# Optimization experiments

Measured on AMD Instinct MI355X. Metric: run time of the kernel, lower is better.

Reference implementation:

```python
import jax, jax.numpy as jnp
import numpy as np

L, B, C, OUT = 4, 4, 256, 4
H, W = 128, 128
HEADS, DH, G = 8, 32, 64
N = H * W
INNER = HEADS * DH
HID = 4 * C


def _ln(x, w, b, eps=1e-5):
    m = jnp.mean(x, -1, keepdims=True)
    v = jnp.mean((x - m) ** 2, -1, keepdims=True)
    return (x - m) / jnp.sqrt(v + eps) * w + b


def setup_inputs() -> dict:
    key = jax.random.key(0)
    ks = iter(jax.random.split(key, 16))
    nrm = lambda shape, s=0.02: jax.random.normal(next(ks), shape, jnp.float32) * s
    return dict(
        fx=jax.random.normal(next(ks), (B, N, C), jnp.float32),
        ln1_w=jnp.ones((L, C)), ln1_b=jnp.zeros((L, C)),
        convx_w=nrm((L, 3, 3, C, INNER)), convx_b=jnp.zeros((L, INNER)),
        convfx_w=nrm((L, 3, 3, C, INNER)), convfx_b=jnp.zeros((L, INNER)),
        slice_w=nrm((L, DH, G)), slice_b=jnp.zeros((L, G)),
        temperature=0.5 * jnp.ones((L, HEADS)),
        wq=nrm((L, DH, DH)), wk=nrm((L, DH, DH)), wv=nrm((L, DH, DH)),
        wo=nrm((L, INNER, C)), bo=jnp.zeros((L, C)),
        ln2_w=jnp.ones((L, C)), ln2_b=jnp.zeros((L, C)),
        w1=nrm((L, C, HID)), b1=jnp.zeros((L, HID)),
        w2=nrm((L, HID, C)), b2=jnp.zeros((L, C)),
        ln3_w=jnp.ones((C,)), ln3_b=jnp.zeros((C,)),
        w_out=nrm((C, OUT)), b_out=jnp.zeros((OUT,)),
    )


def reference(fx, ln1_w, ln1_b, convx_w, convx_b, convfx_w, convfx_b,
              slice_w, slice_b, temperature, wq, wk, wv, wo, bo,
              ln2_w, ln2_b, w1, b1, w2, b2, ln3_w, ln3_b, w_out, b_out):
    Bb = fx.shape[0]
    scale = DH ** -0.5
    for i in range(L):
        # --- Physics attention (slice attention) ---
        x = _ln(fx, ln1_w[i], ln1_b[i])
        ximg = x.reshape(Bb, H, W, C)  # NHWC
        conv = lambda w, b: jax.lax.conv_general_dilated(
            ximg, w, (1, 1), 'SAME',
            dimension_numbers=('NHWC', 'HWIO', 'NHWC')) + b
        fx_mid = conv(convfx_w[i], convfx_b[i]).reshape(Bb, N, HEADS, DH).transpose(0, 2, 1, 3)  # [B,h,N,d]
        x_mid = conv(convx_w[i], convx_b[i]).reshape(Bb, N, HEADS, DH).transpose(0, 2, 1, 3)
        temp = jnp.clip(temperature[i], 0.1, 5.0)[None, :, None, None]
        logits = (jnp.einsum('bhnd,dg->bhng', x_mid, slice_w[i]) + slice_b[i]) / temp
        sw = jax.nn.softmax(logits, axis=-1)  # [B,h,N,G]
        norm = sw.sum(2)  # [B,h,G]
        st = jnp.einsum('bhnc,bhng->bhgc', fx_mid, sw) / (norm + 1e-5)[..., None]  # [B,h,G,d]
        q = jnp.einsum('bhgc,cd->bhgd', st, wq[i])
        k = jnp.einsum('bhgc,cd->bhgd', st, wk[i])
        v = jnp.einsum('bhgc,cd->bhgd', st, wv[i])
        attn = jax.nn.softmax(jnp.einsum('bhgd,bhkd->bhgk', q, k) * scale, axis=-1)
        ot = jnp.einsum('bhgk,bhkd->bhgd', attn, v)  # [B,h,G,d]
        out_x = jnp.einsum('bhgc,bhng->bhnc', ot, sw)  # deslice back to points
        out_x = out_x.transpose(0, 2, 1, 3).reshape(Bb, N, INNER)
        fx = fx + out_x @ wo[i] + bo[i]
        # --- MLP (n_layers=0, no res inside) ---
        h = _ln(fx, ln2_w[i], ln2_b[i])
        h = jax.nn.gelu(h @ w1[i] + b1[i], approximate=False) @ w2[i] + b2[i]
        fx = fx + h
    # last-layer head
    return _ln(fx, ln3_w, ln3_b) @ w_out + b_out
```

## Files before the change

### kernel.cpp

```cpp
#include <hip/hip_runtime.h>
#include <hip/hip_bf16.h>

typedef __hip_bfloat16 bf16;
typedef __bf16 bfv8 __attribute__((ext_vector_type(8)));
typedef float f32x4 __attribute__((ext_vector_type(4)));

#define BB 4
#define HH 128
#define WWI 128
#define NN 16384
#define CC 256
#define LL 4
#define NHEADS 8
#define DHD 32
#define GG 64
#define INNERC 256
#define HIDD 1024
#define SPLIT 32
#define SSP 16

__device__ __forceinline__ float b2f(bf16 x) { return __bfloat162float(x); }
__device__ __forceinline__ bf16 f2b(float x) { return __float2bfloat16(x); }
__device__ __forceinline__ float us2f(unsigned short v) {
  return __uint_as_float(((unsigned)v) << 16);
}

__device__ __forceinline__ void async16(void* l, const void* g) {
  __builtin_amdgcn_global_load_lds(
      (const __attribute__((address_space(1))) void*)g,
      (__attribute__((address_space(3))) void*)l, 16, 0, 0);
}

__device__ __forceinline__ float wave_sum(float v) {
#pragma unroll
  for (int off = 32; off > 0; off >>= 1) v += __shfl_down(v, off, 64);
  return v;
}

__device__ __forceinline__ float gelu_exact(float x) {
  return 0.5f * x * (1.0f + erff(x * 0.70710678118654752f));
}

__global__ void transpose_cast_kernel(const float* __restrict__ src, bf16* __restrict__ dst,
                                      int R, int Cm) {
  __shared__ float tile[32][33];
  int tb = blockIdx.z;
  const float* s = src + (size_t)tb * R * Cm;
  bf16* d = dst + (size_t)tb * R * Cm;
  int c0 = blockIdx.x * 32, r0 = blockIdx.y * 32;
  int tx = threadIdx.x & 31, ty = threadIdx.x >> 5;
  for (int rr = ty; rr < 32; rr += 8) {
    int r = r0 + rr, c = c0 + tx;
    tile[rr][tx] = (r < R && c < Cm) ? s[(size_t)r * Cm + c] : 0.f;
  }
  __syncthreads();
  for (int cc = ty; cc < 32; cc += 8) {
    int c = c0 + cc, r = r0 + tx;
    if (c < Cm && r < R) d[(size_t)c * R + r] = f2b(tile[tx][cc]);
  }
}

__global__ void ln_kernel(const float* __restrict__ x, const float* __restrict__ w,
                          const float* __restrict__ b, bf16* __restrict__ out) {
  int pp = blockIdx.x;
  int t = threadIdx.x;
  float v = x[(size_t)pp * CC + t];
  float s = wave_sum(v);
  float sq = wave_sum(v * v);
  __shared__ float ls[4], lq[4];
  int wid = t >> 6, lane = t & 63;
  if (lane == 0) { ls[wid] = s; lq[wid] = sq; }
  __syncthreads();
  float tot = ls[0] + ls[1] + ls[2] + ls[3];
  float totq = lq[0] + lq[1] + lq[2] + lq[3];
  float mean = tot * (1.0f / CC);
  float var = totq * (1.0f / CC) - mean * mean;
  float rstd = rsqrtf(var + 1e-5f);
  float o = (v - mean) * rstd * w[t] + b[t];
  out[(size_t)pp * CC + t] = f2b(o);
}

__global__ __launch_bounds__(512) void conv_mfma_kernel(
    const bf16* __restrict__ xln, const bf16* __restrict__ wt,
    const float* __restrict__ bias, bf16* __restrict__ out,
    const float* __restrict__ zbuf) {
  __shared__ __align__(16) unsigned short As[3 * 130 * 64];
  __shared__ __align__(16) unsigned short Bsm[2][256 * 64];
  int bid = blockIdx.x;
  bid = (bid & 7) * 64 + (bid >> 3);
  int h = bid & 127;
  int b = bid >> 7;
  int t = threadIdx.x, lane = t & 63, wid = t >> 6;
  int wm = (wid & 1) * 64, wn = (wid >> 1) * 64;
  int l15 = lane & 15, l4 = lane >> 4;
  int wu = t & ~63;
  f32x4 acc[4][4];
#pragma unroll
  for (int mi = 0; mi < 4; ++mi)
#pragma unroll
    for (int ni = 0; ni < 4; ++ni) acc[mi][ni] = (f32x4){0.f, 0.f, 0.f, 0.f};
  const bf16* xbase = xln + (size_t)b * NN * CC;

  for (int q = 0; q < 4; ++q) {
#pragma unroll
    for (int k = 0; k < 6; ++k) {
      int u = t + k * 512;
      int jp = u & 7, pc = u >> 3;
      int r = pc / 130, cl = pc - r * 130;
      int j = jp ^ (cl & 7);
      int gr = h + r - 1, gc = cl - 1;
      const void* src =
          ((unsigned)gr < 128u && (unsigned)gc < 128u)
              ? (const void*)(xbase + ((size_t)(gr * WWI + gc)) * CC + q * 64 + j * 8)
              : (const void*)zbuf;
      async16(&As[(size_t)(wu + k * 512) * 8], src);
    }
    if (t < 48) {
      int u = t + 3072;
      int jp = u & 7, pc = u >> 3;
      int r = pc / 130, cl = pc - r * 130;
      int j = jp ^ (cl & 7);
      int gr = h + r - 1, gc = cl - 1;
      uint4 v = make_uint4(0u, 0u, 0u, 0u);
      if ((unsigned)gr < 128u && (unsigned)gc < 128u)
        v = *(const uint4*)(xbase + ((size_t)(gr * WWI + gc)) * CC + q * 64 + j * 8);
      *(uint4*)(&As[(size_t)u * 8]) = v;
    }
#pragma unroll
    for (int k = 0; k < 4; ++k) {
      int u = t + k * 512;
      int n = u >> 3, jp = u & 7, j = jp ^ (n & 7);
      async16(&Bsm[0][(size_t)(wu + k * 512) * 8],
              wt + (size_t)n * 256 + q * 64 + j * 8);
    }
    __syncthreads();

    for (int tap = 0; tap < 9; ++tap) {
      int cur = tap & 1;
      if (tap < 8) {
#pragma unroll
        for (int k = 0; k < 4; ++k) {
          int u = t + k * 512;
          int n = u >> 3, jp = u & 7, j = jp ^ (n & 7);
          async16(&Bsm[cur ^ 1][(size_t)(wu + k * 512) * 8],
                  wt + ((size_t)((tap + 1) * 256 + n)) * 256 + q * 64 + j * 8);
        }
      }
      int ky = tap / 3, kx = tap - ky * 3;
      const unsigned short* Bc = Bsm[cur];
#pragma unroll
      for (int s = 0; s < 2; ++s) {
        bfv8 af[4], bfr[4];
#pragma unroll
        for (int mi = 0; mi < 4; ++mi) {
          int cl = wm + mi * 16 + l15 + kx;
          af[mi] = *(const bfv8*)(&As[((size_t)(ky * 130 + cl)) * 64 +
                                      (((s * 4 + l4) ^ (cl & 7)) << 3)]);
        }
#pragma unroll
        for (int ni = 0; ni < 4; ++ni) {
          int rn = wn + ni * 16 + l15;
          bfr[ni] = *(const bfv8*)(&Bc[(size_t)rn * 64 + (((s * 4 + l4) ^ (rn & 7)) << 3)]);
        }
#pragma unroll
        for (int mi = 0; mi < 4; ++mi)
#pragma unroll
          for (int ni = 0; ni < 4; ++ni)
            acc[mi][ni] = __builtin_amdgcn_mfma_f32_16x16x32_bf16(af[mi], bfr[ni], acc[mi][ni], 0, 0, 0);
      }
      __syncthreads();
    }
  }
  int colB = wn + l15;
  int rowB = wm + l4 * 4;
#pragma unroll
  for (int ni = 0; ni < 4; ++ni) {
    int oc = colB + ni * 16;
    float bv = bias[oc];
#pragma unroll
    for (int mi = 0; mi < 4; ++mi) {
#pragma unroll
      for (int r = 0; r < 4; ++r) {
        int pix = rowB + mi * 16 + r;
        out[((size_t)(b * NN + h * WWI + pix)) * CC + oc] = f2b(acc[mi][ni][r] + bv);
      }
    }
  }
}

__global__ __launch_bounds__(256, 2) void gemm_acc_kernel(
    const bf16* __restrict__ A, const bf16* __restrict__ BT,
    const float* __restrict__ bias, float* __restrict__ outf,
    int M, int N, int K, size_t strideAz, size_t strideBz, size_t strideOz) {
  A  += (size_t)blockIdx.z * strideAz;
  BT += (size_t)blockIdx.z * strideBz;
  __shared__ __align__(16) unsigned short As[128 * 64];
  __shared__ __align__(16) unsigned short Bs[128 * 64];
  int m0 = blockIdx.x * 128, n0 = blockIdx.y * 128;
  int t = threadIdx.x, lane = t & 63, wid = t >> 6;
  int wm = (wid >> 1) * 64, wn = (wid & 1) * 64;
  int l15 = lane & 15, q4 = lane >> 4;
  int wg = wm >> 4, ng = wn >> 4;
  f32x4 acc[4][4];
#pragma unroll
  for (int mi = 0; mi < 4; ++mi)
#pragma unroll
    for (int ni = 0; ni < 4; ++ni) acc[mi][ni] = (f32x4){0.f, 0.f, 0.f, 0.f};

  for (int kb = 0; kb < K; kb += 64) {
    __syncthreads();
#pragma unroll
    for (int i = 0; i < 4; ++i) {
      int inst = wid * 4 + i;
      int g = inst >> 1, h2 = inst & 1;
      int row = g * 16 + l15;
      int kc = (h2 * 4 + q4) * 8;
      async16(&As[(size_t)g * 1024 + h2 * 512], A + (size_t)(m0 + row) * K + kb + kc);
      async16(&Bs[(size_t)g * 1024 + h2 * 512], BT + (size_t)(n0 + row) * K + kb + kc);
    }
    __syncthreads();
#pragma unroll
    for (int s = 0; s < 2; ++s) {
      int kgrp = s * 4 + q4;
      bfv8 af[4], bfr[4];
#pragma unroll
      for (int mi = 0; mi < 4; ++mi)
        af[mi] = *(const bfv8*)(&As[(size_t)(wg + mi) * 1024 + kgrp * 128 + l15 * 8]);
#pragma unroll
      for (int ni = 0; ni < 4; ++ni)
        bfr[ni] = *(const bfv8*)(&Bs[(size_t)(ng + ni) * 1024 + kgrp * 128 + l15 * 8]);
#pragma unroll
      for (int mi = 0; mi < 4; ++mi)
#pragma unroll
        for (int ni = 0; ni < 4; ++ni)
          acc[mi][ni] = __builtin_amdgcn_mfma_f32_16x16x32_bf16(af[mi], bfr[ni], acc[mi][ni], 0, 0, 0);
    }
  }
  int colB = n0 + wn + l15;
  int rowB = m0 + wm + q4 * 4;
#pragma unroll
  for (int ni = 0; ni < 4; ++ni) {
    int col = colB + ni * 16;
    float bv = bias[col];
#pragma unroll
    for (int mi = 0; mi < 4; ++mi) {
#pragma unroll
      for (int r = 0; r < 4; ++r) {
        int row = rowB + mi * 16 + r;
        outf[(size_t)blockIdx.z * strideOz + (size_t)row * N + col] += acc[mi][ni][r] + bv;
      }
    }
  }
}

__global__ __launch_bounds__(512) void mlp_fused_kernel(
    const bf16* __restrict__ xln, const bf16* __restrict__ w1t,
    const float* __restrict__ b1, const bf16* __restrict__ w2t,
    const float* __restrict__ b2, float* __restrict__ fx) {
  __shared__ __align__(16) unsigned short As[64 * 256];
  __shared__ __align__(16) bf16 Hs[64 * 128];
  __shared__ __align__(16) unsigned short Wb[128 * 256];
  int m0 = blockIdx.x * 64;
  int t = threadIdx.x, lane = t & 63, wid = t >> 6;
  int l15 = lane & 15, q4 = lane >> 4;
  int wm2 = (wid & 1) * 32, wn2 = (wid >> 1) * 32;
  int wm = (wid & 1) * 32, wn = (wid >> 1) * 64;
  int wu = t & ~63;

  const unsigned short* xg = (const unsigned short*)xln + (size_t)m0 * 256;
#pragma unroll
  for (int i = 0; i < 4; ++i) {
    int u = t + i * 512;
    int row = u >> 5;
    int su = (u & ~7) | ((u & 7) ^ (row & 7));
    async16(&As[(size_t)(wu + i * 512) * 8], xg + (size_t)su * 8);
  }
#pragma unroll
  for (int i = 0; i < 8; ++i) {
    int u = t + i * 512;
    int n = u >> 5, v = u & 31;
    int sv = (v & ~7) | ((v & 7) ^ (n & 7));
    async16(&Wb[(size_t)(wu + i * 512) * 8], w1t + (size_t)n * 256 + sv * 8);
  }

  f32x4 accO[2][4];
#pragma unroll
  for (int mi = 0; mi < 2; ++mi)
#pragma unroll
    for (int ni = 0; ni < 4; ++ni) accO[mi][ni] = (f32x4){0.f, 0.f, 0.f, 0.f};
  __syncthreads();

  for (int j = 0; j < 8; ++j) {
    int hbase = j * 128;
    f32x4 acc2[2][2];
#pragma unroll
    for (int mi = 0; mi < 2; ++mi)
#pragma unroll
      for (int nj = 0; nj < 2; ++nj) acc2[mi][nj] = (f32x4){0.f, 0.f, 0.f, 0.f};
#pragma unroll
    for (int kb = 0; kb < 4; ++kb) {
#pragma unroll
      for (int ks = 0; ks < 2; ++ks) {
        int kgrp = ks * 4 + q4;
        bfv8 af[2], bfr[2];
#pragma unroll
        for (int mi = 0; mi < 2; ++mi) {
          int row = wm2 + mi * 16 + l15;
          af[mi] = *(const bfv8*)(&As[row * 256 + kb * 64 + ((kgrp ^ (row & 7)) << 3)]);
        }
#pragma unroll
        for (int nj = 0; nj < 2; ++nj) {
          int n = wn2 + nj * 16 + l15;
          bfr[nj] = *(const bfv8*)(&Wb[n * 256 + kb * 64 + ((kgrp ^ (n & 7)) << 3)]);
        }
#pragma unroll
        for (int mi = 0; mi < 2; ++mi)
#pragma unroll
          for (int nj = 0; nj < 2; ++nj)
            acc2[mi][nj] = __builtin_amdgcn_mfma_f32_16x16x32_bf16(af[mi], bfr[nj], acc2[mi][nj], 0, 0, 0);
      }
    }
    __syncthreads();
#pragma unroll
    for (int i = 0; i < 8; ++i) {
      int u = t + i * 512;
      int n = u >> 4, v = u & 15;
      int sv = (v & ~7) | ((v & 7) ^ (n & 7));
      async16(&Wb[(size_t)(wu + i * 512) * 8], w2t + (size_t)n * 1024 + hbase + sv * 8);
    }
#pragma unroll
    for (int nj = 0; nj < 2; ++nj) {
      int coln = wn2 + nj * 16 + l15;
      float bv = b1[hbase + coln];
      int half = coln >> 6, sub = (coln >> 3) & 7, lo = coln & 7;
#pragma unroll
      for (int mi = 0; mi < 2; ++mi) {
#pragma unroll
        for (int r = 0; r < 4; ++r) {
          int row = wm2 + mi * 16 + q4 * 4 + r;
          float v = acc2[mi][nj][r] + bv;
          Hs[row * 128 + half * 64 + (((sub ^ (row & 7)) << 3) + lo)] = f2b(gelu_exact(v));
        }
      }
    }
    __syncthreads();
#pragma unroll
    for (int kb2 = 0; kb2 < 2; ++kb2) {
#pragma unroll
      for (int ks = 0; ks < 2; ++ks) {
        int kgrp = ks * 4 + q4;
        bfv8 af[2], bfr[4];
#pragma unroll
        for (int mi = 0; mi < 2; ++mi) {
          int row = wm + mi * 16 + l15;
          af[mi] = *(const bfv8*)(&Hs[row * 128 + kb2 * 64 + ((kgrp ^ (row & 7)) << 3)]);
        }
#pragma unroll
        for (int ni = 0; ni < 4; ++ni) {
          int n = wn + ni * 16 + l15;
          bfr[ni] = *(const bfv8*)(&Wb[n * 128 + kb2 * 64 + ((kgrp ^ (n & 7)) << 3)]);
        }
#pragma unroll
        for (int mi = 0; mi < 2; ++mi)
#pragma unroll
          for (int ni = 0; ni < 4; ++ni)
            accO[mi][ni] = __builtin_amdgcn_mfma_f32_16x16x32_bf16(af[mi], bfr[ni], accO[mi][ni], 0, 0, 0);
      }
    }
    if (j < 7) {
      __syncthreads();
#pragma unroll
      for (int i = 0; i < 8; ++i) {
        int u = t + i * 512;
        int n = u >> 5, v = u & 31;
        int sv = (v & ~7) | ((v & 7) ^ (n & 7));
        async16(&Wb[(size_t)(wu + i * 512) * 8],
                w1t + (size_t)(hbase + 128 + n) * 256 + sv * 8);
      }
      __syncthreads();
    }
  }
#pragma unroll
  for (int ni = 0; ni < 4; ++ni) {
    int col = wn + ni * 16 + l15;
    float bv = b2[col];
#pragma unroll
    for (int mi = 0; mi < 2; ++mi) {
#pragma unroll
      for (int r = 0; r < 4; ++r) {
        int row = m0 + wm + mi * 16 + q4 * 4 + r;
        fx[(size_t)row * 256 + col] += accO[mi][ni][r] + bv;
      }
    }
  }
}

__global__ __launch_bounds__(256) void slice_softmax_kernel(
    const bf16* __restrict__ xmid, const float* __restrict__ sw_w,
    const float* __restrict__ sw_b, const float* __restrict__ temp,
    bf16* __restrict__ swout) {
  __shared__ float wsm[32][64];
  __shared__ float xm[SSP][256];
  __shared__ float bias_s[64];
  __shared__ float rtc[8];
  int p0 = blockIdx.x * SSP;
  int t = threadIdx.x;
  for (int i = t; i < 2048; i += 256) wsm[i >> 6][i & 63] = sw_w[i];
  if (t < 64) bias_s[t] = sw_b[t];
  if (t < 8) {
    float x = temp[t];
    rtc[t] = 1.0f / fminf(fmaxf(x, 0.1f), 5.0f);
  }
  const unsigned short* xg = (const unsigned short*)xmid + (size_t)p0 * 256;
#pragma unroll
  for (int i2 = t; i2 < SSP * 32; i2 += 256) {
    uint4 v = ((const uint4*)xg)[i2];
    int p = i2 >> 5, c = (i2 & 31) << 3;
    xm[p][c + 0] = us2f((unsigned short)(v.x & 0xffff));
    xm[p][c + 1] = us2f((unsigned short)(v.x >> 16));
    xm[p][c + 2] = us2f((unsigned short)(v.y & 0xffff));
    xm[p][c + 3] = us2f((unsigned short)(v.y >> 16));
    xm[p][c + 4] = us2f((unsigned short)(v.z & 0xffff));
    xm[p][c + 5] = us2f((unsigned short)(v.z >> 16));
    xm[p][c + 6] = us2f((unsigned short)(v.w & 0xffff));
    xm[p][c + 7] = us2f((unsigned short)(v.w >> 16));
  }
  __syncthreads();
  int g = t & 63, pq = t >> 6;
  for (int pp2 = 0; pp2 < SSP / 4; ++pp2) {
    int p = pp2 * 4 + pq;
#pragma unroll
    for (int h = 0; h < NHEADS; ++h) {
      float acc = bias_s[g];
      const float* xr = &xm[p][h * 32];
#pragma unroll
      for (int d = 0; d < 32; ++d) acc += xr[d] * wsm[d][g];
      float logit = acc * rtc[h];
      float m = logit;
#pragma unroll
      for (int off = 32; off > 0; off >>= 1) m = fmaxf(m, __shfl_xor(m, off, 64));
      float e = __expf(logit - m);
      float s = e;
#pragma unroll
      for (int off = 32; off > 0; off >>= 1) s += __shfl_xor(s, off, 64);
      swout[(size_t)(p0 + p) * 512 + h * 64 + g] = f2b(e / s);
    }
  }
}

__global__ __launch_bounds__(256) void slice_st_kernel(
    const bf16* __restrict__ fxmid, const bf16* __restrict__ sw,
    float* __restrict__ stp, float* __restrict__ normp) {
  __shared__ __align__(16) unsigned short sw_s[64 * 64];
  __shared__ __align__(16) unsigned short fx_s[32 * 64];
  __shared__ float npart[2][64];
  int split = blockIdx.x, h = blockIdx.y, b = blockIdx.z;
  int t = threadIdx.x, w = t >> 6, lane = t & 63;
  int l15 = lane & 15, q4 = lane >> 4;
  int ns0 = split * (NN / SPLIT);
  const int NT = (NN / SPLIT) / 64;
  f32x4 acc0 = {0.f, 0.f, 0.f, 0.f}, acc1 = {0.f, 0.f, 0.f, 0.f};
  float nacc = 0.f;
  const unsigned short* swg = (const unsigned short*)sw + (size_t)b * NN * 512 + h * 64;
  const unsigned short* fxg = (const unsigned short*)fxmid + (size_t)b * NN * 256 + h * 32;

  for (int kt = 0; kt < NT; ++kt) {
    int n0 = ns0 + kt * 64;
    __syncthreads();
    if (w < 2) {
      int g = lane;
#pragma unroll
      for (int i = 0; i < 4; ++i) {
        int j = w + 2 * i;
        const unsigned short* p = swg + (size_t)(n0 + j * 8) * 512 + g;
        unsigned short v0 = p[0],     v1 = p[512],  v2 = p[1024], v3 = p[1536];
        unsigned short v4 = p[2048],  v5 = p[2560], v6 = p[3072], v7 = p[3584];
        nacc += us2f(v0) + us2f(v1) + us2f(v2) + us2f(v3) +
                us2f(v4) + us2f(v5) + us2f(v6) + us2f(v7);
        uint4 pk = make_uint4((unsigned)v0 | ((unsigned)v1 << 16),
                              (unsigned)v2 | ((unsigned)v3 << 16),
                              (unsigned)v4 | ((unsigned)v5 << 16),
                              (unsigned)v6 | ((unsigned)v7 << 16));
        ((uint4*)sw_s)[g * 8 + (j ^ (g & 7))] = pk;
      }
    } else {
      int d = lane & 31, nh = lane >> 5, w3 = w - 2;
#pragma unroll
      for (int i = 0; i < 2; ++i) {
        int nbase = (w3 * 2 + i) * 16 + nh * 8;
        const unsigned short* p = fxg + (size_t)(n0 + nbase) * 256 + d;
        unsigned short v0 = p[0],    v1 = p[256],  v2 = p[512],  v3 = p[768];
        unsigned short v4 = p[1024], v5 = p[1280], v6 = p[1536], v7 = p[1792];
        uint4 pk = make_uint4((unsigned)v0 | ((unsigned)v1 << 16),
                              (unsigned)v2 | ((unsigned)v3 << 16),
                              (unsigned)v4 | ((unsigned)v5 << 16),
                              (unsigned)v6 | ((unsigned)v7 << 16));
        int u = nbase >> 3;
        ((uint4*)fx_s)[d * 8 + (u ^ (d & 7))] = pk;
      }
    }
    __syncthreads();
    int gg = w * 16 + l15;
    int d0 = l15, d1 = 16 + l15;
#pragma unroll
    for (int ks = 0; ks < 2; ++ks) {
      bfv8 af  = ((const bfv8*)sw_s)[gg * 8 + ((ks * 4 + q4) ^ (gg & 7))];
      bfv8 bf0 = ((const bfv8*)fx_s)[d0 * 8 + ((ks * 4 + q4) ^ (d0 & 7))];
      bfv8 bf1 = ((const bfv8*)fx_s)[d1 * 8 + ((ks * 4 + q4) ^ (d1 & 7))];
      acc0 = __builtin_amdgcn_mfma_f32_16x16x32_bf16(af, bf0, acc0, 0, 0, 0);
      acc1 = __builtin_amdgcn_mfma_f32_16x16x32_bf16(af, bf1, acc1, 0, 0, 0);
    }
  }
  if (w < 2) npart[w][lane] = nacc;
  __syncthreads();
  int bh = b * NHEADS + h;
  if (t < 64) normp[(size_t)split * (BB * NHEADS * GG) + bh * 64 + t] = npart[0][t] + npart[1][t];
  size_t base = ((size_t)split * (BB * NHEADS * GG) + bh * 64) * 32;
#pragma unroll
  for (int r = 0; r < 4; ++r) {
    int g = w * 16 + q4 * 4 + r;
    stp[base + (size_t)g * 32 + l15] = acc0[r];
    stp[base + (size_t)g * 32 + 16 + l15] = acc1[r];
  }
}

__global__ __launch_bounds__(256) void attn_kernel(
    const float* __restrict__ stp, const float* __restrict__ normp,
    const float* __restrict__ wq, const float* __restrict__ wk,
    const float* __restrict__ wv, float* __restrict__ ot) {
  __shared__ float wqs[32 * 32], wks[32 * 32], wvs[32 * 32];
  __shared__ float st[GG][DHD + 1];
  __shared__ float qq[GG][DHD + 1], kk[GG][DHD + 1], vv[GG][DHD + 1];
  __shared__ float pm[GG][GG + 1];
  __shared__ float nrm[GG];
  int bh = blockIdx.x;
  int t = threadIdx.x;
  ((float4*)wqs)[t] = ((const float4*)wq)[t];
  ((float4*)wks)[t] = ((const float4*)wk)[t];
  ((float4*)wvs)[t] = ((const float4*)wv)[t];
  if (t < 64) {
    float ns = 0.f;
    for (int s = 0; s < SPLIT; ++s) ns += normp[(size_t)s * (BB * NHEADS * GG) + bh * 64 + t];
    nrm[t] = 1.0f / (ns + 1e-5f);
  }
  __syncthreads();
#pragma unroll
  for (int i = 0; i < 8; ++i) {
    int idx = t + i * 256;
    int g = idx >> 5, d = idx & 31;
    float a = 0.f;
    for (int s = 0; s < SPLIT; ++s)
      a += stp[((size_t)s * (BB * NHEADS * GG) + bh * 64 + g) * 32 + d];
    st[g][d] = a * nrm[g];
  }
  __syncthreads();
#pragma unroll
  for (int i = 0; i < 8; ++i) {
    int idx = t + i * 256;
    int g = idx >> 5, d = idx & 31;
    float aq = 0.f, ak = 0.f, av = 0.f;
#pragma unroll
    for (int c = 0; c < 32; ++c) {
      float sv = st[g][c];
      aq += sv * wqs[c * 32 + d];
      ak += sv * wks[c * 32 + d];
      av += sv * wvs[c * 32 + d];
    }
    qq[g][d] = aq; kk[g][d] = ak; vv[g][d] = av;
  }
  __syncthreads();
  {
    int g = t >> 2, sub = t & 3;
    float sc[16];
    float m = -1e30f;
    const float scale = 0.17677669529663687f;
#pragma unroll
    for (int jj = 0; jj < 16; ++jj) {
      int j = sub * 16 + jj;
      float a = 0.f;
#pragma unroll
      for (int d = 0; d < 32; ++d) a += qq[g][d] * kk[j][d];
      a *= scale;
      sc[jj] = a;
      m = fmaxf(m, a);
    }
    m = fmaxf(m, __shfl_xor(m, 1, 64));
    m = fmaxf(m, __shfl_xor(m, 2, 64));
    float ssum = 0.f;
#pragma unroll
    for (int jj = 0; jj < 16; ++jj) { sc[jj] = __expf(sc[jj] - m); ssum += sc[jj]; }
    ssum += __shfl_xor(ssum, 1, 64);
    ssum += __shfl_xor(ssum, 2, 64);
    float rs = 1.0f / ssum;
#pragma unroll
    for (int jj = 0; jj < 16; ++jj) pm[g][sub * 16 + jj] = sc[jj] * rs;
  }
  __syncthreads();
#pragma unroll
  for (int i = 0; i < 8; ++i) {
    int idx = t + i * 256;
    int g = idx >> 5, d = idx & 31;
    float a = 0.f;
#pragma unroll
    for (int j = 0; j < GG; ++j) a += pm[g][j] * vv[j][d];
    ot[((size_t)bh * GG + g) * DHD + d] = a;
  }
}

__global__ __launch_bounds__(256) void wc_kernel(const float* __restrict__ ot,
                                                 const float* __restrict__ wo,
                                                 bf16* __restrict__ wct) {
  __shared__ float ots[GG][DHD];
  int bh = blockIdx.x;
  int h = bh & 7, b = bh >> 3;
  int t = threadIdx.x;
  for (int i = t; i < GG * DHD; i += 256) ots[i >> 5][i & 31] = ot[(size_t)bh * (GG * DHD) + i];
  float wol[DHD];
#pragma unroll
  for (int d = 0; d < DHD; ++d) wol[d] = wo[(size_t)(h * DHD + d) * CC + t];
  __syncthreads();
  bf16* dst = wct + ((size_t)b * CC + t) * (NHEADS * GG) + h * GG;
#pragma unroll 4
  for (int g = 0; g < GG; ++g) {
    float a = 0.f;
#pragma unroll
    for (int d = 0; d < DHD; ++d) a += wol[d] * ots[g][d];
    dst[g] = f2b(a);
  }
}

__global__ void head_kernel(const float* __restrict__ fx, const float* __restrict__ w,
                            const float* __restrict__ b, const float* __restrict__ wout,
                            const float* __restrict__ bout, float* __restrict__ out) {
  int pp = blockIdx.x;
  int t = threadIdx.x;
  float v = fx[(size_t)pp * CC + t];
  float s = wave_sum(v);
  float sq = wave_sum(v * v);
  __shared__ float ls[4], lq[4];
  int wid = t >> 6, lane = t & 63;
  if (lane == 0) { ls[wid] = s; lq[wid] = sq; }
  __syncthreads();
  float tot = ls[0] + ls[1] + ls[2] + ls[3];
  float totq = lq[0] + lq[1] + lq[2] + lq[3];
  float mean = tot * (1.0f / CC);
  float var = totq * (1.0f / CC) - mean * mean;
  float rstd = rsqrtf(var + 1e-5f);
  float xn = (v - mean) * rstd * w[t] + b[t];
  __shared__ float xs[CC];
  xs[t] = xn;
  __syncthreads();
  if (t < 4) {
    float a = bout[t];
    for (int c = 0; c < CC; ++c) a += xs[c] * wout[c * 4 + t];
    out[(size_t)pp * 4 + t] = a;
  }
}

extern "C" void kernel_launch(void* const* d_in, const int* in_sizes, int n_in,
                              void* d_out, int out_size, void* d_ws, size_t ws_size,
                              hipStream_t stream) {
  const float* fx_in      = (const float*)d_in[0];
  const float* ln1_w      = (const float*)d_in[1];
  const float* ln1_b      = (const float*)d_in[2];
  const float* convx_w    = (const float*)d_in[3];
  const float* convx_b    = (const float*)d_in[4];
  const float* convfx_w   = (const float*)d_in[5];
  const float* convfx_b   = (const float*)d_in[6];
  const float* slice_w    = (const float*)d_in[7];
  const float* slice_b    = (const float*)d_in[8];
  const float* temperature= (const float*)d_in[9];
  const float* wq         = (const float*)d_in[10];
  const float* wk         = (const float*)d_in[11];
  const float* wv         = (const float*)d_in[12];
  const float* wo         = (const float*)d_in[13];
  const float* bo         = (const float*)d_in[14];
  const float* ln2_w      = (const float*)d_in[15];
  const float* ln2_b      = (const float*)d_in[16];
  const float* w1         = (const float*)d_in[17];
  const float* b1         = (const float*)d_in[18];
  const float* w2         = (const float*)d_in[19];
  const float* b2         = (const float*)d_in[20];
  const float* ln3_w      = (const float*)d_in[21];
  const float* ln3_b      = (const float*)d_in[22];
  const float* w_out      = (const float*)d_in[23];
  const float* b_out      = (const float*)d_in[24];
  float* out = (float*)d_out;

  char* ws = (char*)d_ws;
  size_t off = 0;
  auto alloc = [&](size_t bytes) -> void* {
    void* p = ws + off;
    off += (bytes + 255) & ~(size_t)255;
    return p;
  };
  float* fx32  = (float*)alloc((size_t)BB * NN * CC * 4);
  bf16* xln    = (bf16*)alloc((size_t)BB * NN * CC * 2);
  char* uni    = (char*)alloc((size_t)BB * NN * 512 * 2 * 2);
  bf16* xmid   = (bf16*)uni;
  bf16* fxmid  = (bf16*)(uni + (size_t)BB * NN * INNERC * 2);
  bf16* swb    = (bf16*)(uni + (size_t)2 * BB * NN * INNERC * 2);
  float* stp   = (float*)uni;
  float* normp = (float*)(uni + (size_t)SPLIT * BB * NHEADS * GG * DHD * 4);
  bf16* wtx    = (bf16*)alloc((size_t)LL * 9 * CC * INNERC * 2);
  bf16* wtfx   = (bf16*)alloc((size_t)LL * 9 * CC * INNERC * 2);
  bf16* w1t    = (bf16*)alloc((size_t)LL * CC * HIDD * 2);
  bf16* w2t    = (bf16*)alloc((size_t)LL * HIDD * CC * 2);
  float* otb   = (float*)alloc((size_t)BB * NHEADS * GG * DHD * 4);
  bf16* wct    = (bf16*)alloc((size_t)BB * CC * NHEADS * GG * 2);
  float* zbuf  = (float*)alloc(256);
  (void)ws_size; (void)in_sizes; (void)n_in; (void)out_size;

  hipMemsetAsync(zbuf, 0, 256, stream);

  transpose_cast_kernel<<<dim3(8, 8, LL * 9), 256, 0, stream>>>(convx_w, wtx, CC, INNERC);
  transpose_cast_kernel<<<dim3(8, 8, LL * 9), 256, 0, stream>>>(convfx_w, wtfx, CC, INNERC);
  transpose_cast_kernel<<<dim3(32, 8, LL), 256, 0, stream>>>(w1, w1t, CC, HIDD);
  transpose_cast_kernel<<<dim3(8, 32, LL), 256, 0, stream>>>(w2, w2t, HIDD, CC);

  hipMemcpyAsync(fx32, fx_in, (size_t)BB * NN * CC * sizeof(float),
                 hipMemcpyDeviceToDevice, stream);

  const int M = BB * NN;
  for (int i = 0; i < LL; ++i) {
    ln_kernel<<<M, 256, 0, stream>>>(fx32, ln1_w + i * CC, ln1_b + i * CC, xln);
    conv_mfma_kernel<<<BB * HH, 512, 0, stream>>>(
        xln, wtfx + (size_t)i * 9 * CC * INNERC, convfx_b + i * INNERC, fxmid,
        (const float*)zbuf);
    conv_mfma_kernel<<<BB * HH, 512, 0, stream>>>(
        xln, wtx + (size_t)i * 9 * CC * INNERC, convx_b + i * INNERC, xmid,
        (const float*)zbuf);
    slice_softmax_kernel<<<M / SSP, 256, 0, stream>>>(
        xmid, slice_w + i * DHD * GG, slice_b + i * GG, temperature + i * NHEADS, swb);
    slice_st_kernel<<<dim3(SPLIT, NHEADS, BB), 256, 0, stream>>>(fxmid, swb, stp, normp);
    attn_kernel<<<BB * NHEADS, 256, 0, stream>>>(
        stp, normp, wq + i * DHD * DHD, wk + i * DHD * DHD, wv + i * DHD * DHD, otb);
    wc_kernel<<<BB * NHEADS, 256, 0, stream>>>(otb, wo + (size_t)i * INNERC * CC, wct);
    gemm_acc_kernel<<<dim3(NN / 128, CC / 128, BB), 256, 0, stream>>>(
        swb, wct, bo + i * CC, fx32, NN, CC, NHEADS * GG,
        (size_t)NN * (NHEADS * GG), (size_t)CC * (NHEADS * GG), (size_t)NN * CC);
    ln_kernel<<<M, 256, 0, stream>>>(fx32, ln2_w + i * CC, ln2_b + i * CC, xln);
    mlp_fused_kernel<<<M / 64, 512, 0, stream>>>(
        xln, w1t + (size_t)i * CC * HIDD, b1 + i * HIDD,
        w2t + (size_t)i * HIDD * CC, b2 + i * CC, fx32);
  }
  head_kernel<<<M, 256, 0, stream>>>(fx32, ln3_w, ln3_b, w_out, b_out, out);
}
```

Before: 2.763 ms.

## Use wave-per-row LayerNorm/head and shrink MLP weight staging buffer

LayerNorm and the head kernel now handle one row per wave with float4 loads, xor-shuffle reductions and packed bf16 stores, so each block covers four rows and block-level syncs go away. The fused MLP kernel cuts its LDS weight buffer from 128x256 to 256x64, loads weights in 64-wide K chunks through registers with synchronous copies instead of async global-to-LDS loads, and asks for 4 blocks per CU in its launch bounds. The smaller shared memory footprint is meant to raise MLP occupancy, at the cost of more barriers and weight reloads inside the loop that are no longer overlapped with compute.

New measurement: 2.337 ms. -15.4%, faster.

```diff
diff --git a/kernel.cpp b/kernel.cpp
--- a/kernel.cpp
+++ b/kernel.cpp
@@ -24,6 +24,9 @@
 __device__ __forceinline__ float us2f(unsigned short v) {
   return __uint_as_float(((unsigned)v) << 16);
 }
+__device__ __forceinline__ unsigned short b2us(bf16 h) {
+  union { bf16 b; unsigned short u; } c; c.b = h; return c.u;
+}
 
 __device__ __forceinline__ void async16(void* l, const void* g) {
   __builtin_amdgcn_global_load_lds(
@@ -60,24 +63,32 @@
   }
 }
 
-__global__ void ln_kernel(const float* __restrict__ x, const float* __restrict__ w,
-                          const float* __restrict__ b, bf16* __restrict__ out) {
-  int pp = blockIdx.x;
-  int t = threadIdx.x;
-  float v = x[(size_t)pp * CC + t];
-  float s = wave_sum(v);
-  float sq = wave_sum(v * v);
-  __shared__ float ls[4], lq[4];
-  int wid = t >> 6, lane = t & 63;
-  if (lane == 0) { ls[wid] = s; lq[wid] = sq; }
-  __syncthreads();
-  float tot = ls[0] + ls[1] + ls[2] + ls[3];
-  float totq = lq[0] + lq[1] + lq[2] + lq[3];
-  float mean = tot * (1.0f / CC);
-  float var = totq * (1.0f / CC) - mean * mean;
+__global__ __launch_bounds__(256) void ln_kernel(const float* __restrict__ x,
+                                                 const float* __restrict__ w,
+                                                 const float* __restrict__ b,
+                                                 bf16* __restrict__ out) {
+  int wid = threadIdx.x >> 6, lane = threadIdx.x & 63;
+  int p = blockIdx.x * 4 + wid;
+  float4 v = ((const float4*)(x + (size_t)p * CC))[lane];
+  float s = v.x + v.y + v.z + v.w;
+  float sq = v.x * v.x + v.y * v.y + v.z * v.z + v.w * v.w;
+#pragma unroll
+  for (int off = 32; off > 0; off >>= 1) {
+    s += __shfl_xor(s, off, 64);
+    sq += __shfl_xor(sq, off, 64);
+  }
+  float mean = s * (1.0f / CC);
+  float var = sq * (1.0f / CC) - mean * mean;
   float rstd = rsqrtf(var + 1e-5f);
-  float o = (v - mean) * rstd * w[t] + b[t];
-  out[(size_t)pp * CC + t] = f2b(o);
+  float4 wv = ((const float4*)w)[lane];
+  float4 bv = ((const float4*)b)[lane];
+  unsigned short o0 = b2us(f2b((v.x - mean) * rstd * wv.x + bv.x));
+  unsigned short o1 = b2us(f2b((v.y - mean) * rstd * wv.y + bv.y));
+  unsigned short o2 = b2us(f2b((v.z - mean) * rstd * wv.z + bv.z));
+  unsigned short o3 = b2us(f2b((v.w - mean) * rstd * wv.w + bv.w));
+  uint2 pk = make_uint2((unsigned)o0 | ((unsigned)o1 << 16),
+                        (unsigned)o2 | ((unsigned)o3 << 16));
+  ((uint2*)(out + (size_t)p * CC))[lane] = pk;
 }
 
 __global__ __launch_bounds__(512) void conv_mfma_kernel(
@@ -253,34 +264,27 @@
   }
 }
 
-__global__ __launch_bounds__(512) void mlp_fused_kernel(
+__global__ __launch_bounds__(512, 4) void mlp_fused_kernel(
     const bf16* __restrict__ xln, const bf16* __restrict__ w1t,
     const float* __restrict__ b1, const bf16* __restrict__ w2t,
     const float* __restrict__ b2, float* __restrict__ fx) {
   __shared__ __align__(16) unsigned short As[64 * 256];
   __shared__ __align__(16) bf16 Hs[64 * 128];
-  __shared__ __align__(16) unsigned short Wb[128 * 256];
+  __shared__ __align__(16) unsigned short Wb[256 * 64];
   int m0 = blockIdx.x * 64;
   int t = threadIdx.x, lane = t & 63, wid = t >> 6;
   int l15 = lane & 15, q4 = lane >> 4;
   int wm2 = (wid & 1) * 32, wn2 = (wid >> 1) * 32;
   int wm = (wid & 1) * 32, wn = (wid >> 1) * 64;
-  int wu = t & ~63;
 
   const unsigned short* xg = (const unsigned short*)xln + (size_t)m0 * 256;
 #pragma unroll
   for (int i = 0; i < 4; ++i) {
     int u = t + i * 512;
-    int row = u >> 5;
-    int su = (u & ~7) | ((u & 7) ^ (row & 7));
-    async16(&As[(size_t)(wu + i * 512) * 8], xg + (size_t)su * 8);
-  }
-#pragma unroll
-  for (int i = 0; i < 8; ++i) {
-    int u = t + i * 512;
-    int n = u >> 5, v = u & 31;
-    int sv = (v & ~7) | ((v & 7) ^ (n & 7));
-    async16(&Wb[(size_t)(wu + i * 512) * 8], w1t + (size_t)n * 256 + sv * 8);
+    int row = u >> 5, v = u & 31;
+    int kb = v >> 3, jp = v & 7;
+    uint4 val = ((const uint4*)xg)[u];
+    ((uint4*)As)[row * 32 + kb * 8 + (jp ^ (row & 7))] = val;
   }
 
   f32x4 accO[2][4];
@@ -288,7 +292,6 @@
   for (int mi = 0; mi < 2; ++mi)
 #pragma unroll
     for (int ni = 0; ni < 4; ++ni) accO[mi][ni] = (f32x4){0.f, 0.f, 0.f, 0.f};
-  __syncthreads();
 
   for (int j = 0; j < 8; ++j) {
     int hbase = j * 128;
@@ -297,8 +300,16 @@
     for (int mi = 0; mi < 2; ++mi)
 #pragma unroll
       for (int nj = 0; nj < 2; ++nj) acc2[mi][nj] = (f32x4){0.f, 0.f, 0.f, 0.f};
-#pragma unroll
     for (int kb = 0; kb < 4; ++kb) {
+      __syncthreads();
+#pragma unroll
+      for (int i = 0; i < 2; ++i) {
+        int u = t + i * 512;
+        int n = u >> 3, jp = u & 7;
+        uint4 val = *(const uint4*)(w1t + (size_t)(hbase + n) * 256 + kb * 64 + jp * 8);
+        ((uint4*)Wb)[n * 8 + (jp ^ (n & 7))] = val;
+      }
+      __syncthreads();
 #pragma unroll
       for (int ks = 0; ks < 2; ++ks) {
         int kgrp = ks * 4 + q4;
@@ -311,7 +322,7 @@
 #pragma unroll
         for (int nj = 0; nj < 2; ++nj) {
           int n = wn2 + nj * 16 + l15;
-          bfr[nj] = *(const bfv8*)(&Wb[n * 256 + kb * 64 + ((kgrp ^ (n & 7)) << 3)]);
+          bfr[nj] = *(const bfv8*)(&Wb[n * 64 + ((kgrp ^ (n & 7)) << 3)]);
         }
 #pragma unroll
         for (int mi = 0; mi < 2; ++mi)
@@ -319,14 +330,6 @@
           for (int nj = 0; nj < 2; ++nj)
             acc2[mi][nj] = __builtin_amdgcn_mfma_f32_16x16x32_bf16(af[mi], bfr[nj], acc2[mi][nj], 0, 0, 0);
       }
-    }
-    __syncthreads();
-#pragma unroll
-    for (int i = 0; i < 8; ++i) {
-      int u = t + i * 512;
-      int n = u >> 4, v = u & 15;
-      int sv = (v & ~7) | ((v & 7) ^ (n & 7));
-      async16(&Wb[(size_t)(wu + i * 512) * 8], w2t + (size_t)n * 1024 + hbase + sv * 8);
     }
 #pragma unroll
     for (int nj = 0; nj < 2; ++nj) {
@@ -343,9 +346,16 @@
         }
       }
     }
-    __syncthreads();
-#pragma unroll
     for (int kb2 = 0; kb2 < 2; ++kb2) {
+      __syncthreads();
+#pragma unroll
+      for (int i = 0; i < 4; ++i) {
+        int u = t + i * 512;
+        int n = u >> 3, jp = u & 7;
+        uint4 val = *(const uint4*)(w2t + (size_t)n * 1024 + hbase + kb2 * 64 + jp * 8);
+        ((uint4*)Wb)[n * 8 + (jp ^ (n & 7))] = val;
+      }
+      __syncthreads();
 #pragma unroll
       for (int ks = 0; ks < 2; ++ks) {
         int kgrp = ks * 4 + q4;
@@ -358,7 +368,7 @@
 #pragma unroll
         for (int ni = 0; ni < 4; ++ni) {
           int n = wn + ni * 16 + l15;
-          bfr[ni] = *(const bfv8*)(&Wb[n * 128 + kb2 * 64 + ((kgrp ^ (n & 7)) << 3)]);
+          bfr[ni] = *(const bfv8*)(&Wb[n * 64 + ((kgrp ^ (n & 7)) << 3)]);
         }
 #pragma unroll
         for (int mi = 0; mi < 2; ++mi)
@@ -366,18 +376,6 @@
           for (int ni = 0; ni < 4; ++ni)
             accO[mi][ni] = __builtin_amdgcn_mfma_f32_16x16x32_bf16(af[mi], bfr[ni], accO[mi][ni], 0, 0, 0);
       }
-    }
-    if (j < 7) {
-      __syncthreads();
-#pragma unroll
-      for (int i = 0; i < 8; ++i) {
-        int u = t + i * 512;
-        int n = u >> 5, v = u & 31;
-        int sv = (v & ~7) | ((v & 7) ^ (n & 7));
-        async16(&Wb[(size_t)(wu + i * 512) * 8],
-                w1t + (size_t)(hbase + 128 + n) * 256 + sv * 8);
-      }
-      __syncthreads();
     }
   }
 #pragma unroll
@@ -629,31 +627,52 @@
   }
 }
 
-__global__ void head_kernel(const float* __restrict__ fx, const float* __restrict__ w,
-                            const float* __restrict__ b, const float* __restrict__ wout,
-                            const float* __restrict__ bout, float* __restrict__ out) {
-  int pp = blockIdx.x;
-  int t = threadIdx.x;
-  float v = fx[(size_t)pp * CC + t];
-  float s = wave_sum(v);
-  float sq = wave_sum(v * v);
-  __shared__ float ls[4], lq[4];
-  int wid = t >> 6, lane = t & 63;
-  if (lane == 0) { ls[wid] = s; lq[wid] = sq; }
-  __syncthreads();
-  float tot = ls[0] + ls[1] + ls[2] + ls[3];
-  float totq = lq[0] + lq[1] + lq[2] + lq[3];
-  float mean = tot * (1.0f / CC);
-  float var = totq * (1.0f / CC) - mean * mean;
+__global__ __launch_bounds__(256) void head_kernel(const float* __restrict__ fx,
+                                                   const float* __restrict__ w,
+                                                   const float* __restrict__ b,
+                                                   const float* __restrict__ wout,
+                                                   const float* __restrict__ bout,
+                                                   float* __restrict__ out) {
+  int wid = threadIdx.x >> 6, lane = threadIdx.x & 63;
+  int p = blockIdx.x * 4 + wid;
+  float4 v = ((const float4*)(fx + (size_t)p * CC))[lane];
+  float s = v.x + v.y + v.z + v.w;
+  float sq = v.x * v.x + v.y * v.y + v.z * v.z + v.w * v.w;
+#pragma unroll
+  for (int off = 32; off > 0; off >>= 1) {
+    s += __shfl_xor(s, off, 64);
+    sq += __shfl_xor(sq, off, 64);
+  }
+  float mean = s * (1.0f / CC);
+  float var = sq * (1.0f / CC) - mean * mean;
   float rstd = rsqrtf(var + 1e-5f);
-  float xn = (v - mean) * rstd * w[t] + b[t];
-  __shared__ float xs[CC];
-  xs[t] = xn;
-  __syncthreads();
-  if (t < 4) {
-    float a = bout[t];
-    for (int c = 0; c < CC; ++c) a += xs[c] * wout[c * 4 + t];
-    out[(size_t)pp * 4 + t] = a;
+  float4 wv = ((const float4*)w)[lane];
+  float4 bv = ((const float4*)b)[lane];
+  float xn0 = (v.x - mean) * rstd * wv.x + bv.x;
+  float xn1 = (v.y - mean) * rstd * wv.y + bv.y;
+  float xn2 = (v.z - mean) * rstd * wv.z + bv.z;
+  float xn3 = (v.w - mean) * rstd * wv.w + bv.w;
+  float4 w0 = ((const float4*)wout)[lane * 4 + 0];
+  float4 w1 = ((const float4*)wout)[lane * 4 + 1];
+  float4 w2 = ((const float4*)wout)[lane * 4 + 2];
+  float4 w3 = ((const float4*)wout)[lane * 4 + 3];
+  float4 o;
+  o.x = xn0 * w0.x + xn1 * w1.x + xn2 * w2.x + xn3 * w3.x;
+  o.y = xn0 * w0.y + xn1 * w1.y + xn2 * w2.y + xn3 * w3.y;
+  o.z = xn0 * w0.z + xn1 * w1.z + xn2 * w2.z + xn3 * w3.z;
+  o.w = xn0 * w0.w + xn1 * w1.w + xn2 * w2.w + xn3 * w3.w;
+#pragma unroll
+  for (int off = 32; off > 0; off >>= 1) {
+    o.x += __shfl_xor(o.x, off, 64);
+    o.y += __shfl_xor(o.y, off, 64);
+    o.z += __shfl_xor(o.z, off, 64);
+    o.w += __shfl_xor(o.w, off, 64);
+  }
+  if (lane == 0) {
+    float4 bo4 = *((const float4*)bout);
+    float4 r;
+    r.x = o.x + bo4.x; r.y = o.y + bo4.y; r.z = o.z + bo4.z; r.w = o.w + bo4.w;
+    ((float4*)out)[p] = r;
   }
 }
 
@@ -723,7 +742,7 @@
 
   const int M = BB * NN;
   for (int i = 0; i < LL; ++i) {
-    ln_kernel<<<M, 256, 0, stream>>>(fx32, ln1_w + i * CC, ln1_b + i * CC, xln);
+    ln_kernel<<<M / 4, 256, 0, stream>>>(fx32, ln1_w + i * CC, ln1_b + i * CC, xln);
     conv_mfma_kernel<<<BB * HH, 512, 0, stream>>>(
         xln, wtfx + (size_t)i * 9 * CC * INNERC, convfx_b + i * INNERC, fxmid,
         (const float*)zbuf);
@@ -739,10 +758,10 @@
     gemm_acc_kernel<<<dim3(NN / 128, CC / 128, BB), 256, 0, stream>>>(
         swb, wct, bo + i * CC, fx32, NN, CC, NHEADS * GG,
         (size_t)NN * (NHEADS * GG), (size_t)CC * (NHEADS * GG), (size_t)NN * CC);
-    ln_kernel<<<M, 256, 0, stream>>>(fx32, ln2_w + i * CC, ln2_b + i * CC, xln);
+    ln_kernel<<<M / 4, 256, 0, stream>>>(fx32, ln2_w + i * CC, ln2_b + i * CC, xln);
     mlp_fused_kernel<<<M / 64, 512, 0, stream>>>(
         xln, w1t + (size_t)i * CC * HIDD, b1 + i * HIDD,
         w2t + (size_t)i * HIDD * CC, b2 + i * CC, fx32);
   }
-  head_kernel<<<M, 256, 0, stream>>>(fx32, ln3_w, ln3_b, w_out, b_out, out);
-}
+  head_kernel<<<M / 4, 256, 0, stream>>>(fx32, ln3_w, ln3_b, w_out, b_out, out);
+}
```
